# Optimization experiments

Hardware: AMD Instinct MI355X
Metric: run time of the kernel (lower is better)

## Reference

```python
import jax, jax.numpy as jnp
import numpy as np

D = 512        # input_dim
T = 64         # n_trees
DEPTH = 3
NI = 2 ** DEPTH - 1   # 7 internal nodes
NL = 2 ** DEPTH       # 8 leaves
PPT = NI * D + NI + NL * 2   # params per tree
TOT = PPT * T + T            # + tree_weights
HID = 64


def setup_inputs() -> dict:
    key = jax.random.key(0)
    ks = jax.random.split(key, 10)
    w = lambda k, s: jax.random.normal(k, s, jnp.float32) * 0.05  # xavier-ish small gain
    return {
        "X_train": jax.random.normal(ks[0], (8192, D), jnp.float32),
        "X_test": jax.random.normal(ks[1], (32768, D), jnp.float32),
        "y_train": jax.random.randint(ks[2], (8192,), 0, 2, jnp.int64),
        "W1": w(ks[3], (HID, D)), "b1": jnp.zeros(HID), "g1": jnp.ones(HID), "be1": jnp.zeros(HID),
        "W2": w(ks[4], (HID, HID)), "b2": jnp.zeros(HID),
        "H1": w(ks[5], (2 * HID, HID)), "hb1": jnp.zeros(2 * HID),
        "g2": jnp.ones(2 * HID), "be2": jnp.zeros(2 * HID),
        "H2": w(ks[6], (2 * HID, 2 * HID)), "hb2": jnp.zeros(2 * HID),
        "H3": w(ks[7], (TOT, 2 * HID)), "hb3": jnp.zeros(TOT),
    }


def _ln(x, g, b, eps=1e-5):
    m = x.mean(-1, keepdims=True)
    v = ((x - m) ** 2).mean(-1, keepdims=True)
    return (x - m) / jnp.sqrt(v + eps) * g + b


def reference(X_train, X_test, y_train, W1, b1, g1, be1, W2, b2,
              H1, hb1, g2, be2, H2, hb2, H3, hb3):
    # --- hypernet: data encoder + param generator (Dropout is eval=identity) ---
    h = jax.nn.relu(_ln(X_train @ W1.T + b1, g1, be1))
    h = jax.nn.relu(h @ W2.T + b2)
    c = h.mean(axis=0)                              # [HID] context
    u = jax.nn.relu(_ln(c @ H1.T + hb1, g2, be2))
    u = jax.nn.relu(u @ H2.T + hb2)
    params = u @ H3.T + hb3                         # [TOT]

    # --- parse per-tree params (sequential layout) ---
    rows = params[: T * PPT].reshape(T, PPT)
    sw = rows[:, : NI * D].reshape(T, NI, D)        # split weights
    sb = rows[:, NI * D: NI * D + NI]               # split bias [T, NI]
    ll = rows[:, NI * D + NI:].reshape(T, NL, 2)    # leaf logits
    tw = params[T * PPT:]                           # tree weights [T]

    # --- soft decision trees, all trees/nodes batched ---
    # sigmoid split prob for every (sample, tree, internal node); temperature=1
    p = jax.nn.sigmoid(jnp.einsum('bd,tnd->btn', X_test, sw) + sb[None])  # [B,T,NI]
    B = X_test.shape[0]
    lp = jnp.ones((B, T, 1), X_test.dtype)
    for d in range(DEPTH):                          # unrolled fixed-depth traversal
        s = 2 ** d - 1                              # heap offset of level d
        pd = p[:, :, s: s + 2 ** d]                 # [B,T,2^d]
        lp = jnp.stack([lp * (1 - pd), lp * pd], axis=-1).reshape(B, T, 2 ** (d + 1))
    # original code adds leaf contributions twice (main loop + cleanup loop)
    lp = lp * 2.0                                   # [B,T,NL]

    leaf_dist = jax.nn.softmax(ll, axis=-1)         # [T,NL,2]
    out_t = jnp.einsum('btl,tlc->btc', lp, leaf_dist)
    w = jax.nn.softmax(tw, axis=0)                  # [T]
    return jnp.einsum('btc,t->bc', out_t, w)        # [B,2]
```

## Files before the change

### kernel.cpp

```cpp
#include <hip/hip_runtime.h>
#include <hip/hip_bf16.h>

#define DD 512
#define HIDN 64
#define NTREE 64
#define NIN 7
#define PPTC 3607
#define TOTP 230912
#define SWROWS 448

typedef __attribute__((ext_vector_type(8))) short bf16x8;
typedef __attribute__((ext_vector_type(4))) float f32x4;
typedef __attribute__((ext_vector_type(8))) _Float16 h16x8;

__device__ __forceinline__ unsigned short f2bf(float f) {
  unsigned u = __float_as_uint(f);
  unsigned r = (u + 0x7FFFu + ((u >> 16) & 1u)) >> 16;
  return (unsigned short)r;
}
__device__ __forceinline__ float sigmoidf_(float x) {
  return 1.0f / (1.0f + __expf(-x));
}
__device__ __forceinline__ uint2 pack_bf16x4(float4 v) {
  uint2 pk;
  pk.x = (unsigned)f2bf(v.x) | ((unsigned)f2bf(v.y) << 16);
  pk.y = (unsigned)f2bf(v.z) | ((unsigned)f2bf(v.w) << 16);
  return pk;
}
__device__ __forceinline__ uint2 cvtpk2(float4 a) {
  unsigned u0, u1;
  asm("v_cvt_pk_bf16_f32 %0, %1, %2" : "=v"(u0) : "v"(a.x), "v"(a.y));
  asm("v_cvt_pk_bf16_f32 %0, %1, %2" : "=v"(u1) : "v"(a.z), "v"(a.w));
  uint2 r; r.x = u0; r.y = u1;
  return r;
}
__device__ __forceinline__ void gl_lds16(const void* g, void* l) {
  __builtin_amdgcn_global_load_lds(
      (const __attribute__((address_space(1))) unsigned int*)g,
      (__attribute__((address_space(3))) unsigned int*)l, 16, 0, 0);
}

__global__ __launch_bounds__(256) void k_train(
    const float* __restrict__ Xtr, const float* __restrict__ W1,
    const float* __restrict__ b1, const float* __restrict__ g1,
    const float* __restrict__ be1, const float* __restrict__ W2,
    const float* __restrict__ b2, float* __restrict__ c_part)
{
  __shared__ __align__(16) char smem[37888];
  char* Xc  = smem;
  char* W1c = smem + 8192;
  char* Hl  = smem + 24576;
  char* W2l = smem + 28672;
  float* lnb = (float*)(smem + 36864);
  float* cp  = (float*)(smem + 37376);

  const int tid = threadIdx.x;
  const int lane = tid & 63;
  const int wv = tid >> 6;
  const int l15 = lane & 15;
  const int gq = lane >> 4;
  const int wm = wv >> 1;
  const int wn = wv & 1;
  const int rb0 = blockIdx.x * 32;

  const float4* X4g = (const float4*)Xtr;
  const float4* W4g = (const float4*)W1;

#pragma unroll
  for (int s = 0; s < 4; ++s) {
    int fidx = tid + s * 256;
    int n = fidx >> 4, kq = fidx & 15;
    float4 v = ((const float4*)W2)[n * 16 + kq];
    uint2 pk = pack_bf16x4(v);
    int off = n * 128 + kq * 8; off ^= (n & 7) << 4;
    *(uint2*)(W2l + off) = pk;
  }

  int xga[4], xo[4];
#pragma unroll
  for (int s = 0; s < 4; ++s) {
    int f = tid + s * 256;
    int m = f >> 5, kq = f & 31;
    xga[s] = (rb0 + m) * 128 + kq;
    xo[s] = (m * 256 + kq * 8) ^ ((m & 7) << 4);
  }
  int wga[8], wo[8];
#pragma unroll
  for (int s = 0; s < 8; ++s) {
    int f = tid + s * 256;
    int n = f >> 5, kq = f & 31;
    wga[s] = n * 128 + kq;
    wo[s] = (n * 256 + kq * 8) ^ ((n & 7) << 4);
  }

  f32x4 acc1[2];
#pragma unroll
  for (int nt = 0; nt < 2; ++nt) { f32x4 z = {0.f,0.f,0.f,0.f}; acc1[nt] = z; }

  float4 xr[4], wr[8];
#pragma unroll
  for (int s = 0; s < 4; ++s) xr[s] = X4g[xga[s]];
#pragma unroll
  for (int s = 0; s < 8; ++s) wr[s] = W4g[wga[s]];

  for (int kc = 0; kc < 4; ++kc) {
    __syncthreads();
#pragma unroll
    for (int s = 0; s < 4; ++s) *(uint2*)(Xc + xo[s]) = pack_bf16x4(xr[s]);
#pragma unroll
    for (int s = 0; s < 8; ++s) *(uint2*)(W1c + wo[s]) = pack_bf16x4(wr[s]);
    if (kc < 3) {
      int ko = (kc + 1) * 32;
#pragma unroll
      for (int s = 0; s < 4; ++s) xr[s] = X4g[xga[s] + ko];
#pragma unroll
      for (int s = 0; s < 8; ++s) wr[s] = W4g[wga[s] + ko];
    }
    __syncthreads();
#pragma unroll
    for (int ks = 0; ks < 4; ++ks) {
      int arow = wm * 16 + l15;
      int aoff = (arow * 256 + ks * 64 + gq * 16) ^ ((arow & 7) << 4);
      bf16x8 afr = *(const bf16x8*)(Xc + aoff);
#pragma unroll
      for (int nt = 0; nt < 2; ++nt) {
        int brow = wn * 32 + nt * 16 + l15;
        int boff = (brow * 256 + ks * 64 + gq * 16) ^ ((brow & 7) << 4);
        bf16x8 bfr = *(const bf16x8*)(W1c + boff);
        acc1[nt] = __builtin_amdgcn_mfma_f32_16x16x32_bf16(afr, bfr, acc1[nt], 0, 0, 0);
      }
    }
  }

  float b1v[2], g1v[2], be1v[2], b2v[2];
#pragma unroll
  for (int nt = 0; nt < 2; ++nt) {
    int c = wn * 32 + nt * 16 + l15;
    b1v[nt] = b1[c]; g1v[nt] = g1[c]; be1v[nt] = be1[c]; b2v[nt] = b2[c];
  }
  float yv[2][4], s_[4], q_[4];
#pragma unroll
  for (int i = 0; i < 4; ++i) {
    float s = 0.f, q = 0.f;
#pragma unroll
    for (int nt = 0; nt < 2; ++nt) {
      float y = acc1[nt][i] + b1v[nt];
      yv[nt][i] = y; s += y; q += y * y;
    }
    s_[i] = s; q_[i] = q;
  }
#pragma unroll
  for (int off = 1; off < 16; off <<= 1) {
#pragma unroll
    for (int i = 0; i < 4; ++i) {
      s_[i] += __shfl_xor(s_[i], off);
      q_[i] += __shfl_xor(q_[i], off);
    }
  }
  if (l15 == 0) {
#pragma unroll
    for (int i = 0; i < 4; ++i) {
      int row = wm * 16 + gq * 4 + i;
      float2 sv; sv.x = s_[i]; sv.y = q_[i];
      *(float2*)(lnb + (row * 2 + wn) * 2) = sv;
    }
  }
  __syncthreads();
#pragma unroll
  for (int i = 0; i < 4; ++i) {
    int row = wm * 16 + gq * 4 + i;
    float2 e0 = *(float2*)(lnb + (row * 2 + 0) * 2);
    float2 e1 = *(float2*)(lnb + (row * 2 + 1) * 2);
    float m = (e0.x + e1.x) * (1.0f / 64.0f);
    float var = (e0.y + e1.y) * (1.0f / 64.0f) - m * m;
    float rstd = rsqrtf(var + 1e-5f);
#pragma unroll
    for (int nt = 0; nt < 2; ++nt) {
      float h = (yv[nt][i] - m) * rstd * g1v[nt] + be1v[nt];
      h = fmaxf(h, 0.0f);
      int col = wn * 32 + nt * 16 + l15;
      int off2 = (row * 128 + col * 2) ^ ((row & 7) << 4);
      *(unsigned short*)(Hl + off2) = f2bf(h);
    }
  }
  __syncthreads();

  f32x4 acc2[2];
#pragma unroll
  for (int nt = 0; nt < 2; ++nt) { f32x4 z = {0.f,0.f,0.f,0.f}; acc2[nt] = z; }
#pragma unroll
  for (int ks = 0; ks < 2; ++ks) {
    int arow = wm * 16 + l15;
    int aoff = (arow * 128 + ks * 64 + gq * 16) ^ ((arow & 7) << 4);
    bf16x8 afr = *(const bf16x8*)(Hl + aoff);
#pragma unroll
    for (int nt = 0; nt < 2; ++nt) {
      int brow = wn * 32 + nt * 16 + l15;
      int boff = (brow * 128 + ks * 64 + gq * 16) ^ ((brow & 7) << 4);
      bf16x8 bfr = *(const bf16x8*)(W2l + boff);
      acc2[nt] = __builtin_amdgcn_mfma_f32_16x16x32_bf16(afr, bfr, acc2[nt], 0, 0, 0);
    }
  }
  float cs[2];
#pragma unroll
  for (int nt = 0; nt < 2; ++nt) {
    float s = 0.f;
#pragma unroll
    for (int i = 0; i < 4; ++i) s += fmaxf(acc2[nt][i] + b2v[nt], 0.0f);
    cs[nt] = s;
  }
#pragma unroll
  for (int nt = 0; nt < 2; ++nt) {
    cs[nt] += __shfl_xor(cs[nt], 16);
    cs[nt] += __shfl_xor(cs[nt], 32);
  }
  if (lane < 16) {
#pragma unroll
    for (int nt = 0; nt < 2; ++nt)
      cp[wm * 64 + wn * 32 + nt * 16 + lane] = cs[nt];
  }
  __syncthreads();
  if (tid < 64) c_part[blockIdx.x * 64 + tid] = cp[tid] + cp[64 + tid];
}

__global__ __launch_bounds__(256) void k_head(
    const float* __restrict__ c_part,
    const float* __restrict__ H1, const float* __restrict__ hb1,
    const float* __restrict__ g2, const float* __restrict__ be2,
    const float* __restrict__ H2, const float* __restrict__ hb2,
    float* __restrict__ u2out)
{
  __shared__ float part[256];
  __shared__ float clds[64];
  __shared__ float u1lds[128];
  __shared__ float red[8];
  int tid = threadIdx.x;
  {
    int col = tid & 63, g = tid >> 6;
    float s0 = 0.f, s1 = 0.f, s2 = 0.f, s3 = 0.f;
    int b0 = g * 64;
    for (int b = 0; b < 64; b += 4) {
      s0 += c_part[(b0 + b + 0) * 64 + col];
      s1 += c_part[(b0 + b + 1) * 64 + col];
      s2 += c_part[(b0 + b + 2) * 64 + col];
      s3 += c_part[(b0 + b + 3) * 64 + col];
    }
    part[tid] = (s0 + s1) + (s2 + s3);
  }
  __syncthreads();
  if (tid < 64)
    clds[tid] = (part[tid] + part[64 + tid] + part[128 + tid] + part[192 + tid]) * (1.0f / 8192.0f);
  __syncthreads();
  float acc = 0.f;
  if (tid < 128) {
    float a0 = 0.f, a1 = 0.f, a2 = 0.f, a3 = 0.f;
    for (int k = 0; k < 64; k += 4) {
      a0 += clds[k + 0] * H1[tid * 64 + k + 0];
      a1 += clds[k + 1] * H1[tid * 64 + k + 1];
      a2 += clds[k + 2] * H1[tid * 64 + k + 2];
      a3 += clds[k + 3] * H1[tid * 64 + k + 3];
    }
    acc = hb1[tid] + ((a0 + a1) + (a2 + a3));
  }
  float s = acc, q = acc * acc;
#pragma unroll
  for (int off = 1; off < 64; off <<= 1) { s += __shfl_xor(s, off); q += __shfl_xor(q, off); }
  int wv = tid >> 6;
  if ((tid & 63) == 0) { red[wv * 2] = s; red[wv * 2 + 1] = q; }
  __syncthreads();
  float S = red[0] + red[2], Q = red[1] + red[3];
  float m = S * (1.0f / 128.0f);
  float var = Q * (1.0f / 128.0f) - m * m;
  float rstd = rsqrtf(var + 1e-5f);
  if (tid < 128)
    u1lds[tid] = fmaxf((acc - m) * rstd * g2[tid] + be2[tid], 0.0f);
  __syncthreads();
  if (tid < 128) {
    float c0 = 0.f, c1 = 0.f, c2 = 0.f, c3 = 0.f;
    for (int k = 0; k < 128; k += 4) {
      c0 += u1lds[k + 0] * H2[tid * 128 + k + 0];
      c1 += u1lds[k + 1] * H2[tid * 128 + k + 1];
      c2 += u1lds[k + 2] * H2[tid * 128 + k + 2];
      c3 += u1lds[k + 3] * H2[tid * 128 + k + 3];
    }
    u2out[tid] = fmaxf(hb2[tid] + ((c0 + c1) + (c2 + c3)), 0.0f);
  }
}

__global__ __launch_bounds__(256) void k_params(
    const float* __restrict__ H3, const float* __restrict__ hb3,
    const float* __restrict__ u2,
    unsigned short* __restrict__ Bfrag, float* __restrict__ sb,
    float* __restrict__ ll, float* __restrict__ tw)
{
  __shared__ float u2l[128];
  int tid = threadIdx.x;
  if (tid < 128) u2l[tid] = u2[tid];
  __syncthreads();
  int row = blockIdx.x * 64 + (tid >> 2);
  int sub = tid & 3;
  float acc = 0.0f;
  const float4* H4 = (const float4*)H3;
#pragma unroll
  for (int j = 0; j < 8; ++j) {
    int f = j * 4 + sub;
    float4 v = H4[row * 32 + f];
    acc += v.x * u2l[f * 4] + v.y * u2l[f * 4 + 1] + v.z * u2l[f * 4 + 2] + v.w * u2l[f * 4 + 3];
  }
  acc += __shfl_xor(acc, 1);
  acc += __shfl_xor(acc, 2);
  if (sub == 0) {
    float val = acc + hb3[row];
    if (row >= 230848) {
      tw[row - 230848] = val;
    } else {
      int t = row / PPTC;
      int r = row - t * PPTC;
      if (r < 3584) {
        int n = r >> 9, d = r & 511;
        int col = t * 7 + n;
        int kt = d >> 5, kgq = (d >> 3) & 3, j = d & 7;
        Bfrag[kt * 16384 + col * 32 + (kgq ^ ((col >> 1) & 3)) * 8 + j] = f2bf(val);
      } else if (r < 3591) {
        sb[t * 7 + (r - 3584)] = val;
      } else {
        ll[t * 16 + (r - 3591)] = val;
      }
    }
  }
}

__global__ __launch_bounds__(512) void k_test(
    const float* __restrict__ Xt, const unsigned short* __restrict__ Bfrag,
    const float* __restrict__ sb, const float* __restrict__ ll,
    const float* __restrict__ tw, float* __restrict__ out)
{
  __shared__ __align__(16) char smem[121600];
  char* Pl = smem;
  char* Xb0 = smem + 98304;
  char* Xb1 = smem + 106496;
  float* qlds = (float*)(smem + 114688);
  float* sbl  = (float*)(smem + 118784);
  float* outl = (float*)(smem + 120576);

  const int tid = threadIdx.x;
  const int lane = tid & 63;
  const int wv = tid >> 6;
  const int l15 = lane & 15;
  const int gq = lane >> 4;
  const int wm = wv >> 2;
  const int wn = wv & 3;
  const int bm0 = blockIdx.x * 128;

  const float4* X4 = (const float4*)Xt;
  const char* Bf = (const char*)Bfrag;

  if (tid < 448) sbl[tid] = sb[tid];
  if (tid < 64) {
    int t = tid;
    float x = tw[t];
    float m = x;
#pragma unroll
    for (int off = 1; off < 64; off <<= 1) m = fmaxf(m, __shfl_xor(m, off));
    float e = __expf(x - m);
    float s = e;
#pragma unroll
    for (int off = 1; off < 64; off <<= 1) s += __shfl_xor(s, off);
    float w = e / s;
#pragma unroll
    for (int l = 0; l < 8; ++l) {
      float a = ll[t * 16 + l * 2], b = ll[t * 16 + l * 2 + 1];
      float mm = fmaxf(a, b);
      float e0 = __expf(a - mm), e1 = __expf(b - mm);
      float inv = 2.0f * w / (e0 + e1);
      qlds[t * 16 + l * 2] = e0 * inv;
      qlds[t * 16 + l * 2 + 1] = e1 * inv;
    }
  }

  const int xr_ = tid >> 3;
  const int xq_ = tid & 7;
  const int xsrc0 = (bm0 + xr_) * 128 + xq_;
  const int xsrc1 = (bm0 + xr_ + 64) * 128 + xq_;
  const int xwo0 = xr_ * 64 + (((xq_ >> 1) ^ ((xr_ >> 1) & 3)) << 4) + (xq_ & 1) * 8;

  int aoffs[4];
#pragma unroll
  for (int mt = 0; mt < 4; ++mt) {
    int row = wm * 64 + mt * 16 + l15;
    aoffs[mt] = row * 64 + ((gq ^ ((row >> 1) & 3)) << 4);
  }
  int boffs[7];
#pragma unroll
  for (int nt = 0; nt < 7; ++nt) {
    int col = wn * 112 + nt * 16 + l15;
    boffs[nt] = col * 64 + ((gq ^ ((col >> 1) & 3)) << 4);
  }

  f32x4 acc[4][7];
#pragma unroll
  for (int mt = 0; mt < 4; ++mt)
#pragma unroll
    for (int nt = 0; nt < 7; ++nt) { f32x4 z = {0.f,0.f,0.f,0.f}; acc[mt][nt] = z; }

#define LOADX(kt, a_, b_) do { \
    a_ = X4[xsrc0 + (kt) * 8]; b_ = X4[xsrc1 + (kt) * 8]; } while (0)
#define WRITEX(Xb, a_, b_) do { \
    *(uint2*)((Xb) + xwo0) = cvtpk2(a_); \
    *(uint2*)((Xb) + xwo0 + 4096) = cvtpk2(b_); } while (0)
#define ISSUEB(bb, kt) do { \
    const char* bt_ = Bf + (kt) * 32768; \
    gl_lds16(bt_ + tid * 16,          (bb) + tid * 16); \
    gl_lds16(bt_ + tid * 16 + 8192,   (bb) + tid * 16 + 8192); \
    gl_lds16(bt_ + tid * 16 + 16384,  (bb) + tid * 16 + 16384); \
    gl_lds16(bt_ + tid * 16 + 24576,  (bb) + tid * 16 + 24576); } while (0)
#define COMPUTE(Xb, Bb) do { \
    bf16x8 abf[4]; \
    _Pragma("unroll") \
    for (int mt = 0; mt < 4; ++mt) abf[mt] = *(const bf16x8*)((Xb) + aoffs[mt]); \
    _Pragma("unroll") \
    for (int nt = 0; nt < 7; ++nt) { \
      bf16x8 bfr = *(const bf16x8*)((Bb) + boffs[nt]); \
      _Pragma("unroll") \
      for (int mt = 0; mt < 4; ++mt) \
        acc[mt][nt] = __builtin_amdgcn_mfma_f32_16x16x32_bf16(abf[mt], bfr, acc[mt][nt], 0, 0, 0); \
    } } while (0)
#define VMWAIT(n) do { \
    asm volatile("s_waitcnt vmcnt(" #n ")" ::: "memory"); \
    __builtin_amdgcn_sched_barrier(0); } while (0)
#define LGKM0_BAR() do { \
    asm volatile("s_waitcnt lgkmcnt(0)" ::: "memory"); \
    __builtin_amdgcn_s_barrier(); } while (0)

  char* bb0 = smem;
  char* bb1 = smem + 32768;
  char* bb2 = smem + 65536;

  float4 xrA0, xrA1;
  float4 xrB0, xrB1;

  ISSUEB(bb0, 0);
  LOADX(0, xrA0, xrA1);
  __builtin_amdgcn_sched_barrier(0);
  ISSUEB(bb1, 1);
  LOADX(1, xrB0, xrB1);
  __builtin_amdgcn_sched_barrier(0);
  ISSUEB(bb2, 2);
  VMWAIT(10);
  WRITEX(Xb0, xrA0, xrA1);
  LGKM0_BAR();

#pragma unroll 1
  for (int i = 0; i < 6; ++i) {
    const int t = 2 * i;
    COMPUTE(Xb0, bb0);
    VMWAIT(4);
    WRITEX(Xb1, xrB0, xrB1);
    LGKM0_BAR();
    LOADX(t + 2, xrA0, xrA1);
    __builtin_amdgcn_sched_barrier(0);
    ISSUEB(bb0, t + 3);
    COMPUTE(Xb1, bb1);
    VMWAIT(4);
    WRITEX(Xb0, xrA0, xrA1);
    LGKM0_BAR();
    LOADX(t + 3, xrB0, xrB1);
    __builtin_amdgcn_sched_barrier(0);
    ISSUEB(bb1, t + 4);
    char* tmp = bb0; bb0 = bb2; bb2 = bb1; bb1 = tmp;
  }
  COMPUTE(Xb0, bb0);
  VMWAIT(4);
  WRITEX(Xb1, xrB0, xrB1);
  LGKM0_BAR();
  LOADX(14, xrA0, xrA1);
  __builtin_amdgcn_sched_barrier(0);
  ISSUEB(bb0, 15);
  COMPUTE(Xb1, bb1);
  VMWAIT(4);
  WRITEX(Xb0, xrA0, xrA1);
  LGKM0_BAR();
  LOADX(15, xrB0, xrB1);
  __builtin_amdgcn_sched_barrier(0);
  COMPUTE(Xb0, bb2);
  VMWAIT(0);
  WRITEX(Xb1, xrB0, xrB1);
  LGKM0_BAR();
  COMPUTE(Xb1, bb0);
  __syncthreads();

  float qreg[16];
  {
    const float4* q4 = (const float4*)qlds;
#pragma unroll
    for (int j = 0; j < 4; ++j) {
      float4 v = q4[lane * 4 + j];
      qreg[j * 4] = v.x; qreg[j * 4 + 1] = v.y; qreg[j * 4 + 2] = v.z; qreg[j * 4 + 3] = v.w;
    }
  }

#pragma unroll
  for (int rg = 0; rg < 4; ++rg) {
    if (wm == (rg >> 1)) {
#pragma unroll
      for (int mtl = 0; mtl < 2; ++mtl) {
        const int mt = (rg & 1) * 2 + mtl;
#pragma unroll
        for (int nt = 0; nt < 7; ++nt) {
          int col = wn * 112 + nt * 16 + l15;
          float sbv = sbl[col];
          int t = col / 7;
          int j = col - t * 7;
          int slot2 = (t * 8 + j) * 2;
#pragma unroll
          for (int i = 0; i < 4; ++i) {
            int rl = mtl * 16 + gq * 4 + i;
            float p = sigmoidf_(acc[mt][nt][i] + sbv);
            *(_Float16*)(Pl + rl * 1024 + slot2) = (_Float16)p;
          }
        }
      }
    }
    __syncthreads();
#pragma unroll
    for (int k = 0; k < 4; ++k) {
      int rl = wv * 4 + k;
      h16x8 v = *(const h16x8*)(Pl + rl * 1024 + lane * 16);
      float p0 = (float)v[0], p1 = (float)v[1], p2 = (float)v[2];
      float p3 = (float)v[3], p4 = (float)v[4], p5 = (float)v[5], p6 = (float)v[6];
      float n0 = 1.f - p0, n1 = 1.f - p1, n2 = 1.f - p2;
      float a00 = n0 * n1, a01 = n0 * p1, a10 = p0 * n2, a11 = p0 * p2;
      float L0 = a00 * (1.f - p3), L1 = a00 * p3;
      float L2 = a01 * (1.f - p4), L3 = a01 * p4;
      float L4 = a10 * (1.f - p5), L5 = a10 * p5;
      float L6 = a11 * (1.f - p6), L7 = a11 * p6;
      float o0 = L0*qreg[0] + L1*qreg[2] + L2*qreg[4] + L3*qreg[6]
               + L4*qreg[8] + L5*qreg[10] + L6*qreg[12] + L7*qreg[14];
      float o1 = L0*qreg[1] + L1*qreg[3] + L2*qreg[5] + L3*qreg[7]
               + L4*qreg[9] + L5*qreg[11] + L6*qreg[13] + L7*qreg[15];
#pragma unroll
      for (int off = 1; off < 64; off <<= 1) {
        o0 += __shfl_xor(o0, off);
        o1 += __shfl_xor(o1, off);
      }
      if (lane == 0) {
        int gr = rg * 32 + rl;
        outl[gr * 2] = o0;
        outl[gr * 2 + 1] = o1;
      }
    }
    __syncthreads();
  }
  if (tid < 256) out[bm0 * 2 + tid] = outl[tid];
#undef LOADX
#undef WRITEX
#undef ISSUEB
#undef COMPUTE
#undef VMWAIT
#undef LGKM0_BAR
}

extern "C" void kernel_launch(void* const* d_in, const int* in_sizes, int n_in,
                              void* d_out, int out_size, void* d_ws, size_t ws_size,
                              hipStream_t stream)
{
  const float* Xtr = (const float*)d_in[0];
  const float* Xte = (const float*)d_in[1];
  const float* W1  = (const float*)d_in[3];
  const float* b1  = (const float*)d_in[4];
  const float* g1  = (const float*)d_in[5];
  const float* be1 = (const float*)d_in[6];
  const float* W2  = (const float*)d_in[7];
  const float* b2  = (const float*)d_in[8];
  const float* H1  = (const float*)d_in[9];
  const float* hb1 = (const float*)d_in[10];
  const float* g2  = (const float*)d_in[11];
  const float* be2 = (const float*)d_in[12];
  const float* H2  = (const float*)d_in[13];
  const float* hb2 = (const float*)d_in[14];
  const float* H3  = (const float*)d_in[15];
  const float* hb3 = (const float*)d_in[16];
  float* out = (float*)d_out;
  char* ws = (char*)d_ws;

  float* c_part = (float*)ws;
  float* u2     = (float*)(ws + 65536);
  float* sb     = (float*)(ws + 66048);
  float* ll     = (float*)(ws + 67840);
  float* tw     = (float*)(ws + 71936);
  unsigned short* Bfrag = (unsigned short*)(ws + 72192);

  k_train<<<256, 256, 0, stream>>>(Xtr, W1, b1, g1, be1, W2, b2, c_part);
  k_head<<<1, 256, 0, stream>>>(c_part, H1, hb1, g2, be2, H2, hb2, u2);
  k_params<<<3608, 256, 0, stream>>>(H3, hb3, u2, Bfrag, sb, ll, tw);
  k_test<<<256, 512, 0, stream>>>(Xte, Bfrag, sb, ll, tw, out);
}
```

Before: 81.26 us.

## Load B fragments directly into registers instead of staging through LDS

The split-weight B operand is now read straight from global memory into registers, double-buffered across k-steps, replacing the triple-buffered global-to-LDS async copies. The Bfrag layout drops its XOR swizzle, which was only needed for conflict-free LDS reads, and the k_test shared memory footprint shrinks from about 119KB to 55KB, which could allow more blocks per CU. The goal is to cut LDS traffic and LDS capacity pressure. In exchange each wave loads its B fragments itself, possibly with redundant L2 reads across waves, uses more registers, and the prefetch distance is shorter.

```diff
diff --git a/kernel.cpp b/kernel.cpp
--- a/kernel.cpp
+++ b/kernel.cpp
@@ -33,11 +33,6 @@
   asm("v_cvt_pk_bf16_f32 %0, %1, %2" : "=v"(u1) : "v"(a.z), "v"(a.w));
   uint2 r; r.x = u0; r.y = u1;
   return r;
-}
-__device__ __forceinline__ void gl_lds16(const void* g, void* l) {
-  __builtin_amdgcn_global_load_lds(
-      (const __attribute__((address_space(1))) unsigned int*)g,
-      (__attribute__((address_space(3))) unsigned int*)l, 16, 0, 0);
 }
 
 __global__ __launch_bounds__(256) void k_train(
@@ -320,7 +315,7 @@
         int n = r >> 9, d = r & 511;
         int col = t * 7 + n;
         int kt = d >> 5, kgq = (d >> 3) & 3, j = d & 7;
-        Bfrag[kt * 16384 + col * 32 + (kgq ^ ((col >> 1) & 3)) * 8 + j] = f2bf(val);
+        Bfrag[kt * 16384 + col * 32 + kgq * 8 + j] = f2bf(val);
       } else if (r < 3591) {
         sb[t * 7 + (r - 3584)] = val;
       } else {
@@ -335,13 +330,13 @@
     const float* __restrict__ sb, const float* __restrict__ ll,
     const float* __restrict__ tw, float* __restrict__ out)
 {
-  __shared__ __align__(16) char smem[121600];
-  char* Pl = smem;
-  char* Xb0 = smem + 98304;
-  char* Xb1 = smem + 106496;
-  float* qlds = (float*)(smem + 114688);
-  float* sbl  = (float*)(smem + 118784);
-  float* outl = (float*)(smem + 120576);
+  __shared__ __align__(16) char smem[56320];
+  char* Pl  = smem;
+  char* Xb0 = smem + 32768;
+  char* Xb1 = smem + 40960;
+  float* qlds = (float*)(smem + 49152);
+  float* sbl  = (float*)(smem + 53248);
+  float* outl = (float*)(smem + 55040);
 
   const int tid = threadIdx.x;
   const int lane = tid & 63;
@@ -353,7 +348,7 @@
   const int bm0 = blockIdx.x * 128;
 
   const float4* X4 = (const float4*)Xt;
-  const char* Bf = (const char*)Bfrag;
+  const bf16x8* Bf8 = (const bf16x8*)Bfrag;
 
   if (tid < 448) sbl[tid] = sb[tid];
   if (tid < 64) {
@@ -390,12 +385,9 @@
     int row = wm * 64 + mt * 16 + l15;
     aoffs[mt] = row * 64 + ((gq ^ ((row >> 1) & 3)) << 4);
   }
-  int boffs[7];
-#pragma unroll
-  for (int nt = 0; nt < 7; ++nt) {
-    int col = wn * 112 + nt * 16 + l15;
-    boffs[nt] = col * 64 + ((gq ^ ((col >> 1) & 3)) << 4);
-  }
+  int bidx[7];
+#pragma unroll
+  for (int nt = 0; nt < 7; ++nt) bidx[nt] = (wn * 112 + nt * 16 + l15) * 4 + gq;
 
   f32x4 acc[4][7];
 #pragma unroll
@@ -403,27 +395,25 @@
 #pragma unroll
     for (int nt = 0; nt < 7; ++nt) { f32x4 z = {0.f,0.f,0.f,0.f}; acc[mt][nt] = z; }
 
+  bf16x8 B0_[7], B1_[7];
+  float4 xa0, xa1, xb0, xb1;
+
+#define LOADB(Bs, kt) do { _Pragma("unroll") \
+    for (int nt = 0; nt < 7; ++nt) Bs[nt] = Bf8[bidx[nt] + (kt) * 2048]; } while (0)
 #define LOADX(kt, a_, b_) do { \
     a_ = X4[xsrc0 + (kt) * 8]; b_ = X4[xsrc1 + (kt) * 8]; } while (0)
 #define WRITEX(Xb, a_, b_) do { \
     *(uint2*)((Xb) + xwo0) = cvtpk2(a_); \
     *(uint2*)((Xb) + xwo0 + 4096) = cvtpk2(b_); } while (0)
-#define ISSUEB(bb, kt) do { \
-    const char* bt_ = Bf + (kt) * 32768; \
-    gl_lds16(bt_ + tid * 16,          (bb) + tid * 16); \
-    gl_lds16(bt_ + tid * 16 + 8192,   (bb) + tid * 16 + 8192); \
-    gl_lds16(bt_ + tid * 16 + 16384,  (bb) + tid * 16 + 16384); \
-    gl_lds16(bt_ + tid * 16 + 24576,  (bb) + tid * 16 + 24576); } while (0)
-#define COMPUTE(Xb, Bb) do { \
+#define COMPUTE(Xb, Bs) do { \
     bf16x8 abf[4]; \
     _Pragma("unroll") \
     for (int mt = 0; mt < 4; ++mt) abf[mt] = *(const bf16x8*)((Xb) + aoffs[mt]); \
     _Pragma("unroll") \
     for (int nt = 0; nt < 7; ++nt) { \
-      bf16x8 bfr = *(const bf16x8*)((Bb) + boffs[nt]); \
       _Pragma("unroll") \
       for (int mt = 0; mt < 4; ++mt) \
-        acc[mt][nt] = __builtin_amdgcn_mfma_f32_16x16x32_bf16(abf[mt], bfr, acc[mt][nt], 0, 0, 0); \
+        acc[mt][nt] = __builtin_amdgcn_mfma_f32_16x16x32_bf16(abf[mt], Bs[nt], acc[mt][nt], 0, 0, 0); \
     } } while (0)
 #define VMWAIT(n) do { \
     asm volatile("s_waitcnt vmcnt(" #n ")" ::: "memory"); \
@@ -432,61 +422,53 @@
     asm volatile("s_waitcnt lgkmcnt(0)" ::: "memory"); \
     __builtin_amdgcn_s_barrier(); } while (0)
 
-  char* bb0 = smem;
-  char* bb1 = smem + 32768;
-  char* bb2 = smem + 65536;
-
-  float4 xrA0, xrA1;
-  float4 xrB0, xrB1;
-
-  ISSUEB(bb0, 0);
-  LOADX(0, xrA0, xrA1);
+  LOADB(B0_, 0);
+  LOADX(0, xa0, xa1);
   __builtin_amdgcn_sched_barrier(0);
-  ISSUEB(bb1, 1);
-  LOADX(1, xrB0, xrB1);
+  LOADB(B1_, 1);
+  LOADX(1, xb0, xb1);
   __builtin_amdgcn_sched_barrier(0);
-  ISSUEB(bb2, 2);
-  VMWAIT(10);
-  WRITEX(Xb0, xrA0, xrA1);
+  VMWAIT(9);
+  WRITEX(Xb0, xa0, xa1);
   LGKM0_BAR();
 
 #pragma unroll 1
   for (int i = 0; i < 6; ++i) {
     const int t = 2 * i;
-    COMPUTE(Xb0, bb0);
-    VMWAIT(4);
-    WRITEX(Xb1, xrB0, xrB1);
+    COMPUTE(Xb0, B0_);
+    LOADB(B0_, t + 2);
+    LOADX(t + 2, xa0, xa1);
+    __builtin_amdgcn_sched_barrier(0);
+    VMWAIT(9);
+    WRITEX(Xb1, xb0, xb1);
     LGKM0_BAR();
-    LOADX(t + 2, xrA0, xrA1);
+    COMPUTE(Xb1, B1_);
+    LOADB(B1_, t + 3);
+    LOADX(t + 3, xb0, xb1);
     __builtin_amdgcn_sched_barrier(0);
-    ISSUEB(bb0, t + 3);
-    COMPUTE(Xb1, bb1);
-    VMWAIT(4);
-    WRITEX(Xb0, xrA0, xrA1);
+    VMWAIT(9);
+    WRITEX(Xb0, xa0, xa1);
     LGKM0_BAR();
-    LOADX(t + 3, xrB0, xrB1);
-    __builtin_amdgcn_sched_barrier(0);
-    ISSUEB(bb1, t + 4);
-    char* tmp = bb0; bb0 = bb2; bb2 = bb1; bb1 = tmp;
-  }
-  COMPUTE(Xb0, bb0);
-  VMWAIT(4);
-  WRITEX(Xb1, xrB0, xrB1);
+  }
+  COMPUTE(Xb0, B0_);
+  LOADB(B0_, 14);
+  LOADX(14, xa0, xa1);
+  __builtin_amdgcn_sched_barrier(0);
+  VMWAIT(9);
+  WRITEX(Xb1, xb0, xb1);
   LGKM0_BAR();
-  LOADX(14, xrA0, xrA1);
+  COMPUTE(Xb1, B1_);
+  LOADB(B1_, 15);
+  LOADX(15, xb0, xb1);
   __builtin_amdgcn_sched_barrier(0);
-  ISSUEB(bb0, 15);
-  COMPUTE(Xb1, bb1);
-  VMWAIT(4);
-  WRITEX(Xb0, xrA0, xrA1);
+  VMWAIT(9);
+  WRITEX(Xb0, xa0, xa1);
   LGKM0_BAR();
-  LOADX(15, xrB0, xrB1);
-  __builtin_amdgcn_sched_barrier(0);
-  COMPUTE(Xb0, bb2);
+  COMPUTE(Xb0, B0_);
   VMWAIT(0);
-  WRITEX(Xb1, xrB0, xrB1);
+  WRITEX(Xb1, xb0, xb1);
   LGKM0_BAR();
-  COMPUTE(Xb1, bb0);
+  COMPUTE(Xb1, B1_);
   __syncthreads();
 
   float qreg[16];
@@ -552,9 +534,9 @@
     __syncthreads();
   }
   if (tid < 256) out[bm0 * 2 + tid] = outl[tid];
+#undef LOADB
 #undef LOADX
 #undef WRITEX
-#undef ISSUEB
 #undef COMPUTE
 #undef VMWAIT
 #undef LGKM0_BAR
```

Measured after the change: 82.08 us. Within noise of the previous version (+1.0%).
